# Optimization experiments

Hardware: AMD Instinct MI355X
Metric: run time of the kernel (lower is better)

Reference implementation:

```python
import jax, jax.numpy as jnp
import numpy as np

BLOCK_SIZE = 64
WINDOW_SIZE = 512
TOPK_BLOCKS = 16
NEG = -1e30


def setup_inputs() -> dict:
    key = jax.random.key(0)
    ks = jax.random.split(key, 6)
    B, T, D = 4, 8192, 256
    return {
        "queries": jax.random.normal(ks[0], (B, T, D), jnp.float32),
        "keys": jax.random.normal(ks[1], (B, T, D), jnp.float32),
        "values": jax.random.normal(ks[2], (B, T, D), jnp.float32),
        "gate_cmp": jax.random.uniform(ks[3], (B, T), jnp.float32),
        "gate_slc": jax.random.uniform(ks[4], (B, T), jnp.float32),
        "gate_swa": jax.random.uniform(ks[5], (B, T), jnp.float32),
    }


def _compress(x, bs):
    # mean-pool tokens into blocks of size bs (pad tail with zeros like F.pad)
    B, T, D = x.shape
    n_blocks = -(-T // bs)
    pad = n_blocks * bs - T
    if pad > 0:
        x = jnp.pad(x, ((0, 0), (0, pad), (0, 0)))
    return x.reshape(B, n_blocks, bs, D).mean(axis=2)  # [B, n_blocks, D]


def _selective(queries, comp_K, comp_V, gate):
    B, T, D = queries.shape
    nb = comp_K.shape[1]
    scale = D ** -0.5
    scores = jnp.einsum("btd,bnd->btn", queries, comp_K) * scale  # [B,T,nb]
    block_ids = jnp.arange(T) // BLOCK_SIZE                       # query's block
    allowed = jnp.arange(nb)[None, :] <= block_ids[:, None]       # no future blocks
    scores = jnp.where(allowed[None], scores, NEG)
    probs = jax.nn.softmax(scores, axis=-1)
    k = min(TOPK_BLOCKS, nb)
    topk_vals, topk_inds = jax.lax.top_k(probs, k)                # [B,T,k]
    gathered = jax.vmap(lambda cv, idx: cv[idx])(comp_V, topk_inds)  # [B,T,k,D]
    sel = jnp.einsum("btk,btkd->btd", topk_vals, gathered)
    return sel * gate[..., None]


def _sliding(queries, keys, values, gate):
    # block-banded sliding-window attention: each query attends to the last
    # WINDOW_SIZE tokens (inclusive of itself), computed per query-block of
    # size W over a 2W key window [block_start - W, block_end).
    B, T, D = queries.shape
    W = WINDOW_SIZE
    n = T // W
    scale = D ** -0.5
    k_pad = jnp.pad(keys, ((0, 0), (W, 0), (0, 0)))   # [B, T+W, D]
    v_pad = jnp.pad(values, ((0, 0), (W, 0), (0, 0)))
    idx = jnp.arange(n)[:, None] * W + jnp.arange(2 * W)[None, :]  # [n, 2W]
    k_win = k_pad[:, idx]                              # [B, n, 2W, D]
    v_win = v_pad[:, idx]
    q_blk = queries.reshape(B, n, W, D)
    scores = jnp.einsum("bnwd,bncd->bnwc", q_blk, k_win) * scale  # [B,n,W,2W]
    r = jnp.arange(W)[:, None]       # row within block
    c = jnp.arange(2 * W)[None, :]   # col within window
    base = (c <= r + W) & (c >= r + 1)                        # [W, 2W] band
    pos_ok = (jnp.arange(n)[:, None, None] * W + c[None] - W) >= 0  # [n,1,2W]
    mask = base[None] & pos_ok                                 # [n, W, 2W]
    scores = jnp.where(mask[None], scores, NEG)
    attn = jax.nn.softmax(scores, axis=-1)
    out = jnp.einsum("bnwc,bncd->bnwd", attn, v_win).reshape(B, T, D)
    return out * gate[..., None]


def reference(queries, keys, values, gate_cmp, gate_slc, gate_swa):
    D = queries.shape[-1]
    scale = D ** -0.5
    comp_K = _compress(keys, BLOCK_SIZE)
    comp_V = _compress(values, BLOCK_SIZE)
    # compressed branch (note: no causal mask, faithful to the source)
    raw = jnp.einsum("btd,bnd->btn", queries, comp_K) * scale
    comp_out = jnp.einsum("btn,bnd->btd", jax.nn.softmax(raw, axis=-1), comp_V)
    comp_out = comp_out * gate_cmp[..., None]
    sel_out = _selective(queries, comp_K, comp_V, gate_slc)
    slide_out = _sliding(queries, keys, values, gate_swa)
    return comp_out + sel_out + slide_out
```

## Files before the change

### kernel.cpp

```cpp
#include <hip/hip_runtime.h>
#include <hip/hip_bf16.h>

#define Tlen 8192
#define Dd 256
#define NBc 128

typedef __attribute__((ext_vector_type(4))) float f32x4;
typedef __attribute__((ext_vector_type(8))) short bf16x8;

__device__ __forceinline__ unsigned short f2bf(float f){
  unsigned u = __builtin_bit_cast(unsigned, f);
  u += 0x7fffu + ((u >> 16) & 1u);
  return (unsigned short)(u >> 16);
}
__device__ __forceinline__ f32x4 mfma16(bf16x8 a, bf16x8 b, f32x4 c){
  return __builtin_amdgcn_mfma_f32_16x16x32_bf16(a, b, c, 0, 0, 0);
}
__device__ __forceinline__ unsigned pkbf(float a, float b){
  unsigned r; asm("v_cvt_pk_bf16_f32 %0, %1, %2" : "=v"(r) : "v"(a), "v"(b)); return r;
}
__device__ __forceinline__ void bar(){
  asm volatile("" ::: "memory");
  __builtin_amdgcn_s_barrier();
  asm volatile("" ::: "memory");
}
__device__ __forceinline__ bf16x8 pack8(f32x4 a0, f32x4 a1){
  bf16x8 o;
  o[0]=(short)f2bf(a0[0]); o[1]=(short)f2bf(a0[1]); o[2]=(short)f2bf(a0[2]); o[3]=(short)f2bf(a0[3]);
  o[4]=(short)f2bf(a1[0]); o[5]=(short)f2bf(a1[1]); o[6]=(short)f2bf(a1[2]); o[7]=(short)f2bf(a1[3]);
  return o;
}
#define GLL16(g, l) __builtin_amdgcn_global_load_lds( \
    (const __attribute__((address_space(1))) unsigned int*)(const void*)(g), \
    (__attribute__((address_space(3))) unsigned int*)(void*)(l), 16, 0, 0)

template<int C>
__device__ __forceinline__ int dppi(int x){
  return __builtin_amdgcn_update_dpp(x, x, C, 0xF, 0xF, false);
}
template<int C>
__device__ __forceinline__ float dppf(float x){
  return __builtin_bit_cast(float, dppi<C>(__builtin_bit_cast(int, x)));
}
__device__ __forceinline__ float dpp_sum16(float x){
  x += dppf<0x121>(x); x += dppf<0x122>(x); x += dppf<0x124>(x); x += dppf<0x128>(x);
  return x;
}

__device__ __forceinline__ bf16x8 load_qfrag(const float* qrow, int kc, int g){
  f32x4 v0 = *(const f32x4*)(qrow + kc*32 + g*8);
  f32x4 v1 = *(const f32x4*)(qrow + kc*32 + g*8 + 4);
  return pack8(v0, v1);
}

__global__ __launch_bounds__(256) void k_prep(const float* __restrict__ K, const float* __restrict__ V,
    unsigned short* __restrict__ ck, unsigned short* __restrict__ cvt,
    unsigned short* __restrict__ Vswz, unsigned short* __restrict__ Kswz, int do_k){
  __shared__ unsigned short Lt[64][72];
  int b = blockIdx.x >> 7, blk = blockIdx.x & 127;
  int t = threadIdx.x;
  const float* Kb = K + ((size_t)b*Tlen + (size_t)blk*64)*Dd;
  const float* Vb = V + ((size_t)b*Tlen + (size_t)blk*64)*Dd;
  {
    float sk=0.f, sv=0.f;
    #pragma unroll 8
    for (int i=0;i<64;i++){ sk += Kb[(size_t)i*Dd + t]; sv += Vb[(size_t)i*Dd + t]; }
    ck[((size_t)b*NBc + blk)*Dd + (((t>>3) ^ (blk&7))<<3) + (t&7)] = f2bf(sk*(1.f/64.f));
    cvt[((size_t)b*Dd + t)*NBc + blk] = f2bf(sv*(1.f/64.f));
  }
  if (do_k){
    unsigned short* kd = Kswz + ((size_t)(b*NBc + blk))*16384;
    #pragma unroll
    for (int i=0;i<8;i++){
      int id = i*256 + t, r = id>>5, c = id&31;
      f32x4 a0 = *(const f32x4*)(Kb + (size_t)r*Dd + c*8);
      f32x4 a1 = *(const f32x4*)(Kb + (size_t)r*Dd + c*8 + 4);
      *(bf16x8*)(kd + r*256 + ((c ^ (r&7))*8)) = pack8(a0,a1);
    }
  }
  unsigned short* vd = Vswz + ((size_t)(b*NBc + blk))*16384;
  for (int dt=0; dt<4; ++dt){
    __syncthreads();
    #pragma unroll
    for (int it=0; it<4; ++it){
      int idx = it*256 + t, r = idx>>4, c4 = idx&15;
      f32x4 v = *(const f32x4*)(Vb + (size_t)r*Dd + dt*64 + c4*4);
      #pragma unroll
      for (int ii=0;ii<4;ii++) Lt[c4*4+ii][r] = f2bf(v[ii]);
    }
    __syncthreads();
    int dd = t>>2, ch = t&3, d = dt*64 + dd;
    unsigned short tmp[16];
    #pragma unroll
    for (int u=0;u<16;u++) tmp[u] = Lt[dd][ch*16+u];
    *(bf16x8*)(vd + d*64 + (((ch*2  ) ^ (d&7))*8)) = *(bf16x8*)(tmp);
    *(bf16x8*)(vd + d*64 + (((ch*2+1) ^ (d&7))*8)) = *(bf16x8*)(tmp+8);
  }
}

template<bool KPRE>
__device__ __forceinline__ void swa_phase(char* RAW,
    const float* Q, const float* Kf,
    const unsigned short* Kswz, const unsigned short* Vswz,
    const float* gw, int b, int tile, f32x4* po){
  unsigned short* K0 = (unsigned short*)RAW;
  unsigned short* Ps = (unsigned short*)(RAW + 65536);
  float* Lp = (float*)(RAW + 73728);

  int q0 = tile*64;
  int t = threadIdx.x, w = t>>6, l = t&63, g = l>>4, lr = l&15;
  int rg = w & 3;
  int kh = w >> 2;

  bf16x8 qa[8];
  const float* qrow = Q + ((size_t)b*Tlen + q0 + rg*16 + lr)*Dd;
  #pragma unroll
  for (int kc=0;kc<8;kc++) qa[kc] = load_qfrag(qrow, kc, g);

  __syncthreads();
  asm volatile("s_waitcnt vmcnt(0)" ::: "memory");

  #pragma unroll
  for (int i=0;i<8;i++) po[i]=f32x4{0.f,0.f,0.f,0.f};
  float zs[4] = {0.f,0.f,0.f,0.f};

  int jb0 = tile - 8; if (jb0 < 0) jb0 = 0;
  const int jbmax = tile;
  const size_t bof = (size_t)b*NBc*16384;

  auto stage = [&](int buf, int jb){
    const unsigned short* ks = Kswz + bof + (size_t)jb*16384 + t*8;
    #pragma unroll
    for (int i=0;i<4;i++) GLL16(ks + i*4096, &K0[buf*16384 + t*8 + i*4096]);
  };
  int cur = 0;
  if constexpr (KPRE) stage(0, jb0);

  for (int jb = jb0; jb <= jbmax; ++jb){
    if constexpr (KPRE){
      bar();
      if (jb < jbmax){
        stage(cur^1, jb+1);
        asm volatile("s_waitcnt vmcnt(4)" ::: "memory");
      } else {
        asm volatile("s_waitcnt vmcnt(0)" ::: "memory");
      }
      bar();
    } else {
      bar();
      {
        const float* kb = Kf + ((size_t)b*Tlen + (size_t)jb*64)*Dd;
        #pragma unroll
        for (int i=0;i<4;i++){
          int id = i*512 + t, r = id>>5, c = id&31;
          f32x4 a0 = *(const f32x4*)(kb + (size_t)r*Dd + c*8);
          f32x4 a1 = *(const f32x4*)(kb + (size_t)r*Dd + c*8 + 4);
          *(bf16x8*)(&K0[r*256 + ((c ^ (r&7))*8)]) = pack8(a0,a1);
        }
      }
      asm volatile("s_waitcnt vmcnt(0) lgkmcnt(0)" ::: "memory");
      bar();
    }

    f32x4 acc[2];
    acc[0]=f32x4{0.f,0.f,0.f,0.f}; acc[1]=f32x4{0.f,0.f,0.f,0.f};
    #pragma unroll
    for (int nf=0;nf<2;nf++){
      int key = kh*32 + nf*16 + lr;
      const unsigned short* rbase = &K0[cur*16384 + key*256];
      int xk = key & 7;
      #pragma unroll
      for (int kc=0;kc<8;kc++){
        bf16x8 kf = *(const bf16x8*)(rbase + (((kc*4+g) ^ xk)*8));
        acc[nf] = mfma16(qa[kc], kf, acc[nf]);
      }
    }
    #pragma unroll
    for (int nf=0;nf<2;nf++){
      int kloc = kh*32 + nf*16 + lr;
      int kglob = jb*64 + kloc;
      int kchunk = kloc >> 3;
      #pragma unroll
      for (int j=0;j<4;j++){
        int qloc = rg*16 + 4*g + j;
        int qg2 = q0 + qloc;
        float e = (kglob <= qg2 && kglob >= qg2-511) ? __expf(acc[nf][j]*0.0625f) : 0.f;
        zs[j] += e;
        Ps[qloc*64 + ((kchunk ^ (qloc&7))<<3) + (kloc&7)] = f2bf(e);
      }
    }
    asm volatile("s_waitcnt lgkmcnt(0)" ::: "memory");
    bar();

    {
      bf16x8 vf[2][2];
      #pragma unroll
      for (int nf2=0;nf2<2;nf2++){
        int d = w*32 + nf2*16 + lr;
        const unsigned short* vrow = Vswz + bof + (size_t)jb*16384 + (size_t)d*64;
        int xv = d & 7;
        #pragma unroll
        for (int k2=0;k2<2;k2++)
          vf[nf2][k2] = *(const bf16x8*)(vrow + (((k2*4+g) ^ xv)*8));
      }
      #pragma unroll
      for (int rg2=0;rg2<4;rg2++){
        int qloc = rg2*16 + lr;
        int xq = qloc & 7;
        bf16x8 pa0 = *(const bf16x8*)(&Ps[qloc*64 + (((0*4+g) ^ xq)<<3)]);
        bf16x8 pa1 = *(const bf16x8*)(&Ps[qloc*64 + (((1*4+g) ^ xq)<<3)]);
        #pragma unroll
        for (int nf2=0;nf2<2;nf2++){
          po[rg2*2+nf2] = mfma16(pa0, vf[nf2][0], po[rg2*2+nf2]);
          po[rg2*2+nf2] = mfma16(pa1, vf[nf2][1], po[rg2*2+nf2]);
        }
      }
    }
    if constexpr (KPRE) cur ^= 1;
  }

  #pragma unroll
  for (int j=0;j<4;j++) zs[j] = dpp_sum16(zs[j]);
  if (lr == 0){
    #pragma unroll
    for (int j=0;j<4;j++) Lp[kh*64 + rg*16 + 4*g + j] = zs[j];
  }
  __syncthreads();
  #pragma unroll
  for (int rg2=0;rg2<4;rg2++){
    #pragma unroll
    for (int j=0;j<4;j++){
      int qloc = rg2*16 + 4*g + j;
      float scl = gw[(size_t)b*Tlen + q0 + qloc] / (Lp[qloc] + Lp[64 + qloc]);
      #pragma unroll
      for (int nf2=0;nf2<2;nf2++) po[rg2*2+nf2][j] *= scl;
    }
  }
}

__device__ __forceinline__ void compsel_phase(unsigned short* LB,
    const float* Q, const unsigned short* ck, const unsigned short* cvt,
    const float* gc, const float* gs, float* out, int b, int tile, f32x4* po){
  int q0 = tile*64;
  int t = threadIdx.x, w = t >> 6, l = t & 63, g = l >> 4, lr = l & 15;
  int tr = w >> 1, half = w & 1;

  float gcv[2], gsv[2];
  #pragma unroll
  for (int jl=0;jl<2;jl++){
    int qq = q0 + tr*16 + 4*g + half*2 + jl;
    gcv[jl] = gc[(size_t)b*Tlen + qq];
    gsv[jl] = gs[(size_t)b*Tlen + qq];
  }
  bf16x8 qa[8];
  const float* qrow = Q + ((size_t)b*Tlen + q0 + tr*16 + lr)*Dd;
  #pragma unroll
  for (int kc=0;kc<8;kc++) qa[kc] = load_qfrag(qrow, kc, g);

  __syncthreads();

  {
    const unsigned short* src = ck + (size_t)b*NBc*Dd;
    #pragma unroll
    for (int i=0;i<8;i++){
      int idx = i*512 + t;
      GLL16(src + idx*8, &LB[idx*8]);
    }
  }
  asm volatile("s_waitcnt vmcnt(0)" ::: "memory");
  bar();

  f32x4 acc[8];
  #pragma unroll
  for (int nf=0;nf<8;nf++) acc[nf] = f32x4{0.f,0.f,0.f,0.f};
  #pragma unroll
  for (int nf=0;nf<8;nf++){
    int row = nf*16+lr;
    const unsigned short* rbase = &LB[row*256];
    int xk = row & 7;
    #pragma unroll
    for (int kc=0;kc<8;kc++){
      bf16x8 bb = *(const bf16x8*)(rbase + (((kc*4+g) ^ xk)*8));
      acc[nf] = mfma16(qa[kc], bb, acc[nf]);
    }
  }
  #pragma unroll
  for (int nf=0;nf<8;nf++) acc[nf] *= 0.0625f;
  asm volatile("s_waitcnt lgkmcnt(0)" ::: "memory");
  bar();

  bool al[8];
  #pragma unroll
  for (int nf=0;nf<8;nf++) al[nf] = (nf*16+lr) <= tile;

  float e2[8][2];
  #pragma unroll
  for (int nf=0;nf<8;nf++){
    #pragma unroll
    for (int jl=0;jl<2;jl++) e2[nf][jl] = __expf(acc[nf][half*2+jl]);
  }
  float rzc[2], rzs[2];
  {
    float zc2[2]={0.f,0.f}, zs2[2]={0.f,0.f};
    #pragma unroll
    for (int nf=0;nf<8;nf++){
      #pragma unroll
      for (int jl=0;jl<2;jl++){
        zc2[jl] += e2[nf][jl];
        zs2[jl] += al[nf] ? e2[nf][jl] : 0.f;
      }
    }
    #pragma unroll
    for (int jl=0;jl<2;jl++){
      rzc[jl] = 1.f / dpp_sum16(zc2[jl]);
      rzs[jl] = 1.f / dpp_sum16(zs2[jl]);
    }
  }

  float sm2[8][2];
  #pragma unroll
  for (int nf=0;nf<8;nf++){
    #pragma unroll
    for (int jl=0;jl<2;jl++) sm2[nf][jl] = al[nf] ? acc[nf][half*2+jl] : -3e38f;
  }
  unsigned selm[2]={0,0};
  #pragma unroll 1
  for (int it=0; it<16; ++it){
    float bv[2]; int bi[2];
    #pragma unroll
    for (int jl=0;jl<2;jl++){
      float v = sm2[0][jl]; int n = lr;
      #pragma unroll
      for (int nf=1;nf<8;nf++){
        bool tk = sm2[nf][jl] > v;
        v = tk ? sm2[nf][jl] : v;
        n = tk ? nf*16+lr : n;
      }
      bv[jl]=v; bi[jl]=n;
    }
    #define DSTEP(CTRL) \
    _Pragma("unroll") \
    for (int jl=0;jl<2;jl++){ \
      float ov = dppf<CTRL>(bv[jl]); int oi = dppi<CTRL>(bi[jl]); \
      bool tk = (ov>bv[jl]) || (ov==bv[jl] && oi<bi[jl]); \
      bv[jl] = tk ? ov : bv[jl]; bi[jl] = tk ? oi : bi[jl]; \
    }
    DSTEP(0x121) DSTEP(0x122) DSTEP(0x124) DSTEP(0x128)
    #undef DSTEP
    #pragma unroll
    for (int jl=0;jl<2;jl++){
      selm[jl] |= (((bi[jl]&15)==lr) ? (1u<<(bi[jl]>>4)) : 0u);
      #pragma unroll
      for (int nf=0;nf<8;nf++)
        sm2[nf][jl] = (bi[jl] == nf*16+lr) ? -3e38f : sm2[nf][jl];
    }
  }

  unsigned short* Pc = LB;
  #pragma unroll
  for (int nf=0;nf<8;nf++){
    int n = nf*16+lr;
    #pragma unroll
    for (int jl=0;jl<2;jl++){
      float pcm = e2[nf][jl]*rzc[jl];
      float ps  = (al[nf] && ((selm[jl]>>nf)&1u)) ? e2[nf][jl]*rzs[jl] : 0.f;
      Pc[(tr*16 + 4*g + half*2 + jl)*136 + n] = f2bf(gcv[jl]*pcm + gsv[jl]*ps);
    }
  }
  __syncthreads();

  const unsigned short* cvb = cvt + (size_t)b*Dd*NBc;
  bf16x8 vb[2][4];
  #pragma unroll
  for (int nf2=0;nf2<2;nf2++){
    int d = w*32 + nf2*16 + lr;
    #pragma unroll
    for (int kc=0;kc<4;kc++)
      vb[nf2][kc] = *(const bf16x8*)(cvb + (size_t)d*NBc + kc*32 + g*8);
  }
  #pragma unroll
  for (int rg2=0;rg2<4;rg2++){
    bf16x8 pa[4];
    #pragma unroll
    for (int kc=0;kc<4;kc++)
      pa[kc] = *(const bf16x8*)(&Pc[(rg2*16+lr)*136 + kc*32 + g*8]);
    #pragma unroll
    for (int nf2=0;nf2<2;nf2++){
      #pragma unroll
      for (int kc=0;kc<4;kc++)
        po[rg2*2+nf2] = mfma16(pa[kc], vb[nf2][kc], po[rg2*2+nf2]);
    }
  }
  #pragma unroll
  for (int rg2=0;rg2<4;rg2++){
    #pragma unroll
    for (int nf2=0;nf2<2;nf2++){
      #pragma unroll
      for (int j=0;j<4;j++){
        out[((size_t)b*Tlen + q0 + rg2*16 + 4*g + j)*Dd + w*32 + nf2*16 + lr] = po[rg2*2+nf2][j];
      }
    }
  }
}

template<bool KPRE>
__global__ __launch_bounds__(512,4) void k_main(const float* __restrict__ Q, const float* __restrict__ Kf,
    const unsigned short* __restrict__ ck, const unsigned short* __restrict__ cvt,
    const unsigned short* __restrict__ Kswz, const unsigned short* __restrict__ Vswz,
    const float* __restrict__ gc, const float* __restrict__ gs, const float* __restrict__ gw,
    float* __restrict__ out, int nt){
  __shared__ __align__(16) char RAW[74240];
  int wg = blockIdx.x;
  int lin = ((nt & 7) == 0) ? ((wg & 7)*(nt >> 3) + (wg >> 3)) : wg;
  int b = lin >> 7, tile = lin & 127;
  f32x4 po[8];
  swa_phase<KPRE>(RAW, Q, Kf, Kswz, Vswz, gw, b, tile, po);
  compsel_phase((unsigned short*)RAW, Q, ck, cvt, gc, gs, out, b, tile, po);
}

extern "C" void kernel_launch(void* const* d_in, const int* in_sizes, int n_in,
                              void* d_out, int out_size, void* d_ws, size_t ws_size,
                              hipStream_t stream) {
  const float* Q  = (const float*)d_in[0];
  const float* K  = (const float*)d_in[1];
  const float* V  = (const float*)d_in[2];
  const float* gc = (const float*)d_in[3];
  const float* gs = (const float*)d_in[4];
  const float* gwp= (const float*)d_in[5];
  float* out = (float*)d_out;
  int B = in_sizes[0] / (Tlen*Dd);

  unsigned short* ck  = (unsigned short*)d_ws;
  unsigned short* cvt = ck  + (size_t)B*NBc*Dd;
  unsigned short* Vsw = cvt + (size_t)B*Dd*NBc;
  unsigned short* Ksw = Vsw + (size_t)B*Tlen*Dd;

  size_t need_full = ((size_t)B*((size_t)NBc*Dd + (size_t)Dd*NBc + 2*(size_t)Tlen*Dd))*2;
  bool kpre = ws_size >= need_full;
  int nt = B*128;

  k_prep<<<dim3(B*128), dim3(256), 0, stream>>>(K, V, ck, cvt, Vsw, Ksw, kpre?1:0);
  if (kpre) k_main<true ><<<dim3(nt), dim3(512), 0, stream>>>(Q, K, ck, cvt, Ksw, Vsw, gc, gs, gwp, out, nt);
  else      k_main<false><<<dim3(nt), dim3(512), 0, stream>>>(Q, K, ck, cvt, Ksw, Vsw, gc, gs, gwp, out, nt);
}
```

Baseline: 109.5 us.

## Shrink LDS footprint by dropping K double-buffer and halving compressed-key staging

Removes double buffering of K tiles in the sliding-window phase so each block loads into a single buffer and waits for completion before compute. The compressed-key staging in the comp/sel phase now loads 64 rows at a time in two passes instead of all 128 at once. The Lp scratch area reuses the Ps region. Total shared memory drops from about 74 KB to 40 KB, which lets more workgroups fit per CU, at the cost of losing load/compute overlap within a block and adding extra barriers.

```diff
diff --git a/kernel.cpp b/kernel.cpp
--- a/kernel.cpp
+++ b/kernel.cpp
@@ -15,9 +15,6 @@
 }
 __device__ __forceinline__ f32x4 mfma16(bf16x8 a, bf16x8 b, f32x4 c){
   return __builtin_amdgcn_mfma_f32_16x16x32_bf16(a, b, c, 0, 0, 0);
-}
-__device__ __forceinline__ unsigned pkbf(float a, float b){
-  unsigned r; asm("v_cvt_pk_bf16_f32 %0, %1, %2" : "=v"(r) : "v"(a), "v"(b)); return r;
 }
 __device__ __forceinline__ void bar(){
   asm volatile("" ::: "memory");
@@ -104,8 +101,7 @@
     const unsigned short* Kswz, const unsigned short* Vswz,
     const float* gw, int b, int tile, f32x4* po){
   unsigned short* K0 = (unsigned short*)RAW;
-  unsigned short* Ps = (unsigned short*)(RAW + 65536);
-  float* Lp = (float*)(RAW + 73728);
+  unsigned short* Ps = (unsigned short*)(RAW + 32768);
 
   int q0 = tile*64;
   int t = threadIdx.x, w = t>>6, l = t&63, g = l>>4, lr = l&15;
@@ -117,9 +113,6 @@
   #pragma unroll
   for (int kc=0;kc<8;kc++) qa[kc] = load_qfrag(qrow, kc, g);
 
-  __syncthreads();
-  asm volatile("s_waitcnt vmcnt(0)" ::: "memory");
-
   #pragma unroll
   for (int i=0;i<8;i++) po[i]=f32x4{0.f,0.f,0.f,0.f};
   float zs[4] = {0.f,0.f,0.f,0.f};
@@ -128,46 +121,32 @@
   const int jbmax = tile;
   const size_t bof = (size_t)b*NBc*16384;
 
-  auto stage = [&](int buf, int jb){
-    const unsigned short* ks = Kswz + bof + (size_t)jb*16384 + t*8;
-    #pragma unroll
-    for (int i=0;i<4;i++) GLL16(ks + i*4096, &K0[buf*16384 + t*8 + i*4096]);
-  };
-  int cur = 0;
-  if constexpr (KPRE) stage(0, jb0);
-
   for (int jb = jb0; jb <= jbmax; ++jb){
+    bar();
     if constexpr (KPRE){
-      bar();
-      if (jb < jbmax){
-        stage(cur^1, jb+1);
-        asm volatile("s_waitcnt vmcnt(4)" ::: "memory");
-      } else {
-        asm volatile("s_waitcnt vmcnt(0)" ::: "memory");
-      }
-      bar();
+      const unsigned short* ks = Kswz + bof + (size_t)jb*16384 + t*8;
+      #pragma unroll
+      for (int i=0;i<4;i++) GLL16(ks + i*4096, &K0[t*8 + i*4096]);
+      asm volatile("s_waitcnt vmcnt(0)" ::: "memory");
     } else {
-      bar();
-      {
-        const float* kb = Kf + ((size_t)b*Tlen + (size_t)jb*64)*Dd;
-        #pragma unroll
-        for (int i=0;i<4;i++){
-          int id = i*512 + t, r = id>>5, c = id&31;
-          f32x4 a0 = *(const f32x4*)(kb + (size_t)r*Dd + c*8);
-          f32x4 a1 = *(const f32x4*)(kb + (size_t)r*Dd + c*8 + 4);
-          *(bf16x8*)(&K0[r*256 + ((c ^ (r&7))*8)]) = pack8(a0,a1);
-        }
+      const float* kb = Kf + ((size_t)b*Tlen + (size_t)jb*64)*Dd;
+      #pragma unroll
+      for (int i=0;i<4;i++){
+        int id = i*512 + t, r = id>>5, c = id&31;
+        f32x4 a0 = *(const f32x4*)(kb + (size_t)r*Dd + c*8);
+        f32x4 a1 = *(const f32x4*)(kb + (size_t)r*Dd + c*8 + 4);
+        *(bf16x8*)(&K0[r*256 + ((c ^ (r&7))*8)]) = pack8(a0,a1);
       }
       asm volatile("s_waitcnt vmcnt(0) lgkmcnt(0)" ::: "memory");
-      bar();
-    }
+    }
+    bar();
 
     f32x4 acc[2];
     acc[0]=f32x4{0.f,0.f,0.f,0.f}; acc[1]=f32x4{0.f,0.f,0.f,0.f};
     #pragma unroll
     for (int nf=0;nf<2;nf++){
       int key = kh*32 + nf*16 + lr;
-      const unsigned short* rbase = &K0[cur*16384 + key*256];
+      const unsigned short* rbase = &K0[key*256];
       int xk = key & 7;
       #pragma unroll
       for (int kc=0;kc<8;kc++){
@@ -216,9 +195,10 @@
         }
       }
     }
-    if constexpr (KPRE) cur ^= 1;
-  }
-
+  }
+
+  bar();
+  float* Lp = (float*)Ps;
   #pragma unroll
   for (int j=0;j<4;j++) zs[j] = dpp_sum16(zs[j]);
   if (lr == 0){
@@ -259,35 +239,36 @@
 
   __syncthreads();
 
-  {
-    const unsigned short* src = ck + (size_t)b*NBc*Dd;
-    #pragma unroll
-    for (int i=0;i<8;i++){
+  f32x4 acc[8];
+  #pragma unroll
+  for (int nf=0;nf<8;nf++) acc[nf] = f32x4{0.f,0.f,0.f,0.f};
+  #pragma unroll 1
+  for (int h=0; h<2; ++h){
+    const unsigned short* src = ck + (size_t)b*NBc*Dd + (size_t)h*64*Dd;
+    #pragma unroll
+    for (int i=0;i<4;i++){
       int idx = i*512 + t;
       GLL16(src + idx*8, &LB[idx*8]);
     }
-  }
-  asm volatile("s_waitcnt vmcnt(0)" ::: "memory");
-  bar();
-
-  f32x4 acc[8];
-  #pragma unroll
-  for (int nf=0;nf<8;nf++) acc[nf] = f32x4{0.f,0.f,0.f,0.f};
-  #pragma unroll
-  for (int nf=0;nf<8;nf++){
-    int row = nf*16+lr;
-    const unsigned short* rbase = &LB[row*256];
-    int xk = row & 7;
-    #pragma unroll
-    for (int kc=0;kc<8;kc++){
-      bf16x8 bb = *(const bf16x8*)(rbase + (((kc*4+g) ^ xk)*8));
-      acc[nf] = mfma16(qa[kc], bb, acc[nf]);
-    }
+    asm volatile("s_waitcnt vmcnt(0)" ::: "memory");
+    bar();
+    #pragma unroll
+    for (int nl=0;nl<4;nl++){
+      int nf = h*4 + nl;
+      int lrow = nl*16+lr;
+      const unsigned short* rbase = &LB[lrow*256];
+      int xk = lrow & 7;
+      #pragma unroll
+      for (int kc=0;kc<8;kc++){
+        bf16x8 bb = *(const bf16x8*)(rbase + (((kc*4+g) ^ xk)*8));
+        acc[nf] = mfma16(qa[kc], bb, acc[nf]);
+      }
+    }
+    asm volatile("s_waitcnt lgkmcnt(0)" ::: "memory");
+    bar();
   }
   #pragma unroll
   for (int nf=0;nf<8;nf++) acc[nf] *= 0.0625f;
-  asm volatile("s_waitcnt lgkmcnt(0)" ::: "memory");
-  bar();
 
   bool al[8];
   #pragma unroll
@@ -409,7 +390,7 @@
     const unsigned short* __restrict__ Kswz, const unsigned short* __restrict__ Vswz,
     const float* __restrict__ gc, const float* __restrict__ gs, const float* __restrict__ gw,
     float* __restrict__ out, int nt){
-  __shared__ __align__(16) char RAW[74240];
+  __shared__ __align__(16) char RAW[40960];
   int wg = blockIdx.x;
   int lin = ((nt & 7) == 0) ? ((wg & 7)*(nt >> 3) + (wg >> 3)) : wg;
   int b = lin >> 7, tile = lin & 127;
```

Result: slower. 128.3 us (+17.2%).
